# Performance work log

Measured on AMD Instinct MI355X. Metric: run time of the kernel, lower is better.

Reference implementation:

```python
import jax, jax.numpy as jnp
import numpy as np

B, C, H, Wd = 16, 512, 56, 56
WCH = 128  # W_ch: projection rank of phi/rou


def setup_inputs() -> dict:
    key = jax.random.key(0)
    ks = jax.random.split(key, 8)
    s = 0.02
    return {
        "x": jax.random.normal(ks[0], (B, C, H, Wd), dtype=jnp.float32),
        "y": jax.random.normal(ks[1], (B, C, H, Wd), dtype=jnp.float32),
        # phi: Conv2d(C, WCH, 1) -> weight [WCH, C], bias [WCH]
        "phi_w": jax.random.normal(ks[2], (WCH, C), dtype=jnp.float32) * s,
        "phi_b": jnp.zeros((WCH,), dtype=jnp.float32),
        # rou: Conv2d(C, WCH, 1) applied to globally pooled y -> acts as Linear
        "rou_w": jax.random.normal(ks[3], (WCH, C), dtype=jnp.float32) * s,
        "rou_b": jnp.zeros((WCH,), dtype=jnp.float32),
        # zeta: Linear(C, C)
        "zeta_w": jax.random.normal(ks[4], (C, C), dtype=jnp.float32) * s,
        "zeta_b": jnp.zeros((C,), dtype=jnp.float32),
    }


def reference(x, y, phi_w, phi_b, rou_w, rou_b, zeta_w, zeta_b):
    b, c, h, w = x.shape
    hw = h * w
    # phi_xT = relu(phi(x)).view(B, WCH, HW); phi_x = transpose -> [B, HW, WCH]
    phi_xT = jax.nn.relu(jnp.einsum('kc,bchw->bkhw', phi_w, x) + phi_b[None, :, None, None])
    phi_x = phi_xT.reshape(b, -1, hw).transpose(0, 2, 1)  # [B, HW, WCH]
    # rou_y = sigmoid(rou(global_avg_pool(y))) -> [B, WCH]
    pooled = y.mean(axis=(2, 3))  # [B, C]
    rou_y = jax.nn.sigmoid(pooled @ rou_w.T + rou_b)  # [B, WCH]
    # D_i = sum_j (phi_x diag(rou) phi_x^T)_{ij} = sum_k phi_x[i,k] rou[k] s[k]
    s = phi_x.sum(axis=1)  # [B, WCH], column sums
    D = jnp.einsum('bnk,bk,bk->bn', phi_x, rou_y, s)  # [B, HW]
    inv_sqrt = 1.0 / jnp.sqrt(D + 1e-8)
    P = phi_x * inv_sqrt[..., None]  # diag(D^-1/2) @ phi_x, [B, HW, WCH]
    # x.view(B, -1, C): raw row-major reshape of [B,C,H,W] (NOT a transpose)
    x_trans = x.reshape(b, hw, c)
    # LX = x_trans - P diag(rou) P^T x_trans, re-associated right-to-left
    t = jnp.einsum('bnk,bnc->bkc', P, x_trans)          # P^T x_trans, [B, WCH, C]
    LX = x_trans - jnp.einsum('bnk,bk,bkc->bnc', P, rou_y, t)
    # zeta Linear + dropout(eval: identity) + relu, residual add
    out = jax.nn.relu(LX @ zeta_w.T + zeta_b)
    return x + out.reshape(b, c, h, w)
```

## Files before the change

### kernel.cpp

```cpp
#include <hip/hip_runtime.h>
#include <math.h>

#define B_  16
#define C_  512
#define HW_ 3136
#define K_  128
#define CHW (C_ * HW_)

typedef __bf16 bf16x8_t __attribute__((ext_vector_type(8)));
typedef __bf16 bf16x4_t __attribute__((ext_vector_type(4)));
typedef __bf16 bf16x2_t __attribute__((ext_vector_type(2)));
typedef float floatx4  __attribute__((ext_vector_type(4)));

typedef const __attribute__((address_space(1))) void* gas_ptr;
typedef __attribute__((address_space(3))) void*       las_ptr;

static __device__ __forceinline__ unsigned short bfbits(__bf16 v) {
    return __builtin_bit_cast(unsigned short, v);
}

__device__ __forceinline__ void stage128x64(const __bf16* __restrict__ base, long ld,
                                            int row0, int rowmax, int k0,
                                            __bf16* lds, int t) {
    int w = t >> 6;
    #pragma unroll
    for (int i = 0; i < 4; ++i) {
        int u = i * 256 + t;
        int m = u >> 3, slot = u & 7;
        int kg = slot ^ (m & 7);
        int r = row0 + m; if (r > rowmax) r = rowmax;
        const __bf16* g = base + (long)r * ld + (k0 + kg * 8);
        __bf16* l = lds + (size_t)(i * 256 + w * 64) * 8;
        __builtin_amdgcn_global_load_lds((gas_ptr)g, (las_ptr)l, 16, 0, 0);
    }
}

__device__ __forceinline__ void stage_tr_phi(const __bf16* __restrict__ src,
                                             int n0, int p0, char* Bs, int t) {
    int ng = t & 15;
    int cp2 = (t >> 4) * 2;
    #pragma unroll
    for (int ci = 0; ci < 2; ++ci) {
        int cc = cp2 + ci * 32;
        const __bf16* g0 = src + (long)(p0 + cc) * HW_ + n0 + ng * 8;
        bf16x8_t v0 = *(const bf16x8_t*)g0;
        bf16x8_t v1 = *(const bf16x8_t*)(g0 + HW_);
        int r8 = cc >> 3, sub = (cc & 7) >> 1;
        #pragma unroll
        for (int j = 0; j < 8; ++j) {
            int row = ng * 8 + j;
            int slot = (r8 + row + (row >> 3)) & 7;
            unsigned int pr = ((unsigned int)bfbits(v1[j]) << 16) | bfbits(v0[j]);
            *(unsigned int*)(Bs + row * 144 + slot * 16 + sub * 4) = pr;
        }
    }
}

__device__ __forceinline__ void stage_tr_t(const __bf16* __restrict__ src,
                                           const float* __restrict__ isrc,
                                           int c0, int p0, char* Bs, int t) {
    int cg = t & 15;
    int np2 = (t >> 4) * 2;
    #pragma unroll
    for (int ni = 0; ni < 2; ++ni) {
        int nn = np2 + ni * 32;
        int n = p0 + nn;
        float s0 = isrc[n], s1 = isrc[n + 1];
        const __bf16* g0 = src + (long)n * C_ + c0 + cg * 8;
        bf16x8_t v0 = *(const bf16x8_t*)g0;
        bf16x8_t v1 = *(const bf16x8_t*)(g0 + C_);
        int r8 = nn >> 3, sub = (nn & 7) >> 1;
        #pragma unroll
        for (int j = 0; j < 8; ++j) {
            int row = cg * 8 + j;
            int slot = (r8 + row + (row >> 3)) & 7;
            __bf16 a0 = (__bf16)((float)v0[j] * s0);
            __bf16 a1 = (__bf16)((float)v1[j] * s1);
            unsigned int pr = ((unsigned int)bfbits(a1) << 16) | bfbits(a0);
            *(unsigned int*)(Bs + row * 144 + slot * 16 + sub * 4) = pr;
        }
    }
}

__device__ __forceinline__ void mma_step64(const char* As, const char* Bs,
                                           floatx4 acc[4][4], int aoff, int boff,
                                           int q, int lxor) {
    #pragma unroll
    for (int h = 0; h < 2; ++h) {
        int s = (((h * 4 + q) ^ lxor) << 4);
        bf16x8_t af[4], bf[4];
        #pragma unroll
        for (int i = 0; i < 4; ++i) af[i] = *(const bf16x8_t*)(As + aoff + i * 2048 + s);
        #pragma unroll
        for (int i = 0; i < 4; ++i) bf[i] = *(const bf16x8_t*)(Bs + boff + i * 2048 + s);
        #pragma unroll
        for (int mi = 0; mi < 4; ++mi)
            #pragma unroll
            for (int ni = 0; ni < 4; ++ni)
                acc[mi][ni] = __builtin_amdgcn_mfma_f32_16x16x32_bf16(af[mi], bf[ni], acc[mi][ni], 0, 0, 0);
    }
}

__device__ __forceinline__ void mma_step_mix(const char* As, const char* Bs,
                                             floatx4 acc[4][4], int lm, int q,
                                             int wrow, int wcol) {
    int lxor = lm & 7;
    int aoff = (wrow * 64 + lm) * 128;
    #pragma unroll
    for (int h = 0; h < 2; ++h) {
        int g = h * 4 + q;
        int sa = (g ^ lxor) << 4;
        bf16x8_t af[4], bf[4];
        #pragma unroll
        for (int i = 0; i < 4; ++i) af[i] = *(const bf16x8_t*)(As + aoff + i * 2048 + sa);
        #pragma unroll
        for (int i = 0; i < 4; ++i) {
            int brow = wcol * 64 + i * 16 + lm;
            int slot = (g + brow + (brow >> 3)) & 7;
            bf[i] = *(const bf16x8_t*)(Bs + brow * 144 + slot * 16);
        }
        #pragma unroll
        for (int mi = 0; mi < 4; ++mi)
            #pragma unroll
            for (int ni = 0; ni < 4; ++ni)
                acc[mi][ni] = __builtin_amdgcn_mfma_f32_16x16x32_bf16(af[mi], bf[ni], acc[mi][ni], 0, 0, 0);
    }
}


__global__ __launch_bounds__(256) void k_pool(const float* __restrict__ y,
                                              float* __restrict__ pooled) {
    int bc = blockIdx.x;
    const float* yp = y + (long)bc * HW_;
    float acc = 0.f;
    for (int n = threadIdx.x; n < HW_; n += 256) acc += yp[n];
    __shared__ float red[256];
    red[threadIdx.x] = acc;
    __syncthreads();
    for (int s = 128; s > 0; s >>= 1) {
        if (threadIdx.x < s) red[threadIdx.x] += red[threadIdx.x + s];
        __syncthreads();
    }
    if (threadIdx.x == 0) pooled[bc] = red[0] * (1.0f / HW_);
}

__global__ __launch_bounds__(128) void k_rou(const float* __restrict__ pooled,
                                             const float* __restrict__ rou_w,
                                             const float* __restrict__ rou_b,
                                             float* __restrict__ rou_y) {
    int b = blockIdx.x;
    int k = threadIdx.x;
    __shared__ float ps[C_];
    for (int c = threadIdx.x; c < C_; c += 128) ps[c] = pooled[b * C_ + c];
    __syncthreads();
    float acc = rou_b[k];
    for (int c = 0; c < C_; ++c) acc += ps[c] * rou_w[k * C_ + c];
    rou_y[b * K_ + k] = 1.0f / (1.0f + expf(-acc));
}

__global__ __launch_bounds__(256) void k_cast8(const float* __restrict__ a,
                                               __bf16* __restrict__ o) {
    long i = ((long)blockIdx.x * 256 + threadIdx.x) * 8;
    float4 v0 = *reinterpret_cast<const float4*>(a + i);
    float4 v1 = *reinterpret_cast<const float4*>(a + i + 4);
    bf16x8_t r;
    r[0] = (__bf16)v0.x; r[1] = (__bf16)v0.y; r[2] = (__bf16)v0.z; r[3] = (__bf16)v0.w;
    r[4] = (__bf16)v1.x; r[5] = (__bf16)v1.y; r[6] = (__bf16)v1.z; r[7] = (__bf16)v1.w;
    *reinterpret_cast<bf16x8_t*>(o + i) = r;
}


__global__ __launch_bounds__(256) void k_phi_m(const __bf16* __restrict__ xbf2,
                                               const __bf16* __restrict__ pwbf,
                                               const float* __restrict__ phi_b,
                                               __bf16* __restrict__ phi_kn,
                                               __bf16* __restrict__ phi_nk,
                                               float* __restrict__ sbuf) {
    int b = blockIdx.y;
    int n0 = blockIdx.x * 128;
    __shared__ __attribute__((aligned(16))) char smem[16384 + 18432];
    char* As = smem; char* Bs = smem + 16384;
    int t = threadIdx.x, w = t >> 6, lane = t & 63;
    int lm = lane & 15, q = lane >> 4;
    int wrow = w >> 1, wcol = w & 1;
    floatx4 acc[4][4];
    #pragma unroll
    for (int i = 0; i < 4; ++i)
        #pragma unroll
        for (int j = 0; j < 4; ++j) acc[i][j] = (floatx4){0.f, 0.f, 0.f, 0.f};

    const __bf16* Bb = xbf2 + (long)b * CHW;
    for (int p0 = 0; p0 < C_; p0 += 64) {
        stage128x64(pwbf, C_, 0, K_ - 1, p0, (__bf16*)As, t);
        stage_tr_phi(Bb, n0, p0, Bs, t);
        __syncthreads();
        mma_step_mix(As, Bs, acc, lm, q, wrow, wcol);
        __syncthreads();
    }
    #pragma unroll
    for (int mi = 0; mi < 4; ++mi) {
        int kb = wrow * 64 + mi * 16 + q * 4;
        float4 pb = *reinterpret_cast<const float4*>(phi_b + kb);
        float pbv[4] = {pb.x, pb.y, pb.z, pb.w};
        float sv[4] = {0.f, 0.f, 0.f, 0.f};
        #pragma unroll
        for (int ni = 0; ni < 4; ++ni) {
            int n = n0 + wcol * 64 + ni * 16 + lm;
            if (n < HW_) {
                bf16x4_t pack;
                #pragma unroll
                for (int r = 0; r < 4; ++r) {
                    float v = fmaxf(acc[mi][ni][r] + pbv[r], 0.f);
                    __bf16 vb = (__bf16)v;
                    phi_kn[((long)b * K_ + kb + r) * HW_ + n] = vb;
                    pack[r] = vb;
                    sv[r] += v;
                }
                *reinterpret_cast<bf16x4_t*>(phi_nk + ((long)b * HW_ + n) * K_ + kb) = pack;
            }
        }
        #pragma unroll
        for (int r = 0; r < 4; ++r) {
            float v = sv[r];
            v += __shfl_xor(v, 1, 64); v += __shfl_xor(v, 2, 64);
            v += __shfl_xor(v, 4, 64); v += __shfl_xor(v, 8, 64);
            if (lm == 0) atomicAdd(&sbuf[b * K_ + kb + r], v);
        }
    }
}

__global__ __launch_bounds__(256) void k_d2(__bf16* __restrict__ phi_nk,
                                            const float* __restrict__ rou_y,
                                            const float* __restrict__ s,
                                            float* __restrict__ inv_s) {
    int b = blockIdx.y;
    __shared__ float ws[K_];
    int t = threadIdx.x;
    if (t < K_) ws[t] = rou_y[b * K_ + t] * s[b * K_ + t];
    __syncthreads();
    int w = t >> 6, lane = t & 63;
    int n = blockIdx.x * 4 + w;
    __bf16* p = phi_nk + ((long)b * HW_ + n) * K_ + lane * 2;
    bf16x2_t v = *reinterpret_cast<bf16x2_t*>(p);
    float f0 = (float)v[0], f1 = (float)v[1];
    float d = f0 * ws[lane * 2] + f1 * ws[lane * 2 + 1];
    #pragma unroll
    for (int off = 32; off > 0; off >>= 1) d += __shfl_xor(d, off, 64);
    float inv = rsqrtf(d + 1e-8f);
    bf16x2_t o; o[0] = (__bf16)(f0 * inv); o[1] = (__bf16)(f1 * inv);
    *reinterpret_cast<bf16x2_t*>(p) = o;
    if (lane == 0) inv_s[b * HW_ + n] = inv;
}

__global__ __launch_bounds__(256) void k_t_m(const __bf16* __restrict__ phi_kn,
                                             const __bf16* __restrict__ xbf2,
                                             const float* __restrict__ inv_s,
                                             float* __restrict__ t_part) {
    int gid = blockIdx.x;
    int rlo = gid & 7, cc4 = (gid >> 3) & 3, r8 = gid >> 5;
    int r = r8 * 8 + rlo;
    int b = r / 7, nch = r % 7;
    int c0 = cc4 * 128;
    __shared__ __attribute__((aligned(16))) char smem[16384 + 18432];
    char* As = smem; char* Bs = smem + 16384;
    int t = threadIdx.x, w = t >> 6, lane = t & 63;
    int lm = lane & 15, q = lane >> 4;
    int wrow = w >> 1, wcol = w & 1;
    floatx4 acc[4][4];
    #pragma unroll
    for (int i = 0; i < 4; ++i)
        #pragma unroll
        for (int j = 0; j < 4; ++j) acc[i][j] = (floatx4){0.f, 0.f, 0.f, 0.f};

    const __bf16* Ab = phi_kn + (long)b * K_ * HW_;
    const __bf16* Bb = xbf2 + (long)b * CHW;
    const float* ib = inv_s + (long)b * HW_;

    int pstart = nch * 448;
    for (int p0 = pstart; p0 < pstart + 448; p0 += 64) {
        stage128x64(Ab, HW_, 0, K_ - 1, p0, (__bf16*)As, t);
        stage_tr_t(Bb, ib, c0, p0, Bs, t);
        __syncthreads();
        mma_step_mix(As, Bs, acc, lm, q, wrow, wcol);
        __syncthreads();
    }
    float* outp = t_part + ((long)nch * B_ + b) * K_ * C_;
    #pragma unroll
    for (int mi = 0; mi < 4; ++mi) {
        int kb = wrow * 64 + mi * 16 + q * 4;
        #pragma unroll
        for (int ni = 0; ni < 4; ++ni) {
            int c = c0 + wcol * 64 + ni * 16 + lm;
            #pragma unroll
            for (int rr = 0; rr < 4; ++rr)
                outp[(long)(kb + rr) * C_ + c] = acc[mi][ni][rr];
        }
    }
}

__global__ __launch_bounds__(256) void k_tred(const float* __restrict__ t_part,
                                              __bf16* __restrict__ t_bf) {
    const long BKC = (long)B_ * K_ * C_;
    long i = ((long)blockIdx.x * 256 + threadIdx.x) * 4;
    float4 s = *reinterpret_cast<const float4*>(t_part + i);
    #pragma unroll
    for (int p = 1; p < 7; ++p) {
        float4 v = *reinterpret_cast<const float4*>(t_part + p * BKC + i);
        s.x += v.x; s.y += v.y; s.z += v.z; s.w += v.w;
    }
    bf16x4_t o;
    o[0] = (__bf16)s.x; o[1] = (__bf16)s.y; o[2] = (__bf16)s.z; o[3] = (__bf16)s.w;
    *reinterpret_cast<bf16x4_t*>(t_bf + i) = o;
}

__global__ __launch_bounds__(256) void k_tz_m(const __bf16* __restrict__ zwbf,
                                              const __bf16* __restrict__ t_bf,
                                              const float* __restrict__ rou_y,
                                              __bf16* __restrict__ tzT) {
    int b = blockIdx.y;
    int c0 = blockIdx.x * 128;
    __shared__ __attribute__((aligned(16))) char smem[32768];
    char* As = smem; char* Bs = smem + 16384;
    int t = threadIdx.x, w = t >> 6, lane = t & 63;
    int lm = lane & 15, q = lane >> 4;
    int wrow = w >> 1, wcol = w & 1;
    floatx4 acc[4][4];
    #pragma unroll
    for (int i = 0; i < 4; ++i)
        #pragma unroll
        for (int j = 0; j < 4; ++j) acc[i][j] = (floatx4){0.f, 0.f, 0.f, 0.f};

    const __bf16* Bb = t_bf + (long)b * K_ * C_;
    int lxor = lm & 7;
    int aoff = (wrow * 64 + lm) * 128;
    int boff = (wcol * 64 + lm) * 128;

    for (int p0 = 0; p0 < C_; p0 += 64) {
        stage128x64(zwbf, C_, c0, C_ - 1, p0, (__bf16*)As, t);
        stage128x64(Bb,   C_, 0, K_ - 1, p0, (__bf16*)Bs, t);
        __syncthreads();
        mma_step64(As, Bs, acc, aoff, boff, q, lxor);
        __syncthreads();
    }
    #pragma unroll
    for (int mi = 0; mi < 4; ++mi) {
        int c = c0 + wrow * 64 + mi * 16 + q * 4;
        #pragma unroll
        for (int ni = 0; ni < 4; ++ni) {
            int k = wcol * 64 + ni * 16 + lm;
            float rk = rou_y[b * K_ + k];
            #pragma unroll
            for (int rr = 0; rr < 4; ++rr)
                tzT[((long)b * C_ + c + rr) * K_ + k] = (__bf16)(-rk * acc[mi][ni][rr]);
        }
    }
}

__global__ __launch_bounds__(256) void k_out_m(const __bf16* __restrict__ xbf2,
                                               const __bf16* __restrict__ zwbf,
                                               const __bf16* __restrict__ pnk,
                                               const __bf16* __restrict__ tzT,
                                               const float* __restrict__ zeta_b,
                                               float* __restrict__ out) {
    int gid = blockIdx.x;
    int rlo = gid & 7, cc4 = (gid >> 3) & 3, r8 = gid >> 5;
    int r = r8 * 8 + rlo;
    int b = r / 25, nt = r % 25;
    int n0 = nt * 128;
    int c0 = cc4 * 128;
    __shared__ __attribute__((aligned(16))) char smem[32768];
    char* As = smem; char* Bs = smem + 16384;
    int t = threadIdx.x, w = t >> 6, lane = t & 63;
    int lm = lane & 15, q = lane >> 4;
    int wrow = w >> 1, wcol = w & 1;
    floatx4 acc[4][4];
    #pragma unroll
    for (int i = 0; i < 4; ++i)
        #pragma unroll
        for (int j = 0; j < 4; ++j) acc[i][j] = (floatx4){0.f, 0.f, 0.f, 0.f};

    int lxor = lm & 7;
    int aoff = (wrow * 64 + lm) * 128;
    int boff = (wcol * 64 + lm) * 128;

    const __bf16* A1 = xbf2 + (long)b * CHW;
    for (int p0 = 0; p0 < C_; p0 += 64) {
        stage128x64(A1,   C_, n0, HW_ - 1, p0, (__bf16*)As, t);
        stage128x64(zwbf, C_, c0, C_ - 1, p0, (__bf16*)Bs, t);
        __syncthreads();
        mma_step64(As, Bs, acc, aoff, boff, q, lxor);
        __syncthreads();
    }
    const __bf16* A2 = pnk + (long)b * (long)HW_ * K_;
    const __bf16* B2 = tzT + (long)b * (long)C_ * K_;
    for (int p0 = 0; p0 < K_; p0 += 64) {
        stage128x64(A2, K_, n0, HW_ - 1, p0, (__bf16*)As, t);
        stage128x64(B2, K_, c0, C_ - 1, p0, (__bf16*)Bs, t);
        __syncthreads();
        mma_step64(As, Bs, acc, aoff, boff, q, lxor);
        __syncthreads();
    }
    float* ep = (float*)smem;
    const __bf16* xres = xbf2 + (long)b * CHW;
    int lr = t >> 3, lc = (t & 7) * 16;
    #pragma unroll
    for (int ch = 0; ch < 4; ++ch) {
        __syncthreads();
        if (wrow == (ch >> 1)) {
            #pragma unroll
            for (int mm = 0; mm < 2; ++mm) {
                int mi = (ch & 1) * 2 + mm;
                #pragma unroll
                for (int ni = 0; ni < 4; ++ni)
                    #pragma unroll
                    for (int rr = 0; rr < 4; ++rr)
                        ep[(mm * 16 + q * 4 + rr) * 132 + wcol * 64 + ni * 16 + lm] = acc[mi][ni][rr];
            }
        }
        __syncthreads();
        int n = n0 + ch * 32 + lr;
        if (n < HW_) {
            long rowbase = (long)n * C_ + c0 + lc;
            bf16x8_t x0 = *(const bf16x8_t*)(xres + rowbase);
            bf16x8_t x1 = *(const bf16x8_t*)(xres + rowbase + 8);
            float xv[16];
            #pragma unroll
            for (int j = 0; j < 8; ++j) { xv[j] = (float)x0[j]; xv[8 + j] = (float)x1[j]; }
            float* orow = out + (long)b * CHW + rowbase;
            #pragma unroll
            for (int jj = 0; jj < 4; ++jj) {
                float4 zb = *reinterpret_cast<const float4*>(zeta_b + c0 + lc + jj * 4);
                float4 e  = *reinterpret_cast<const float4*>(&ep[lr * 132 + lc + jj * 4]);
                float4 o;
                o.x = xv[jj * 4 + 0] + fmaxf(e.x + zb.x, 0.f);
                o.y = xv[jj * 4 + 1] + fmaxf(e.y + zb.y, 0.f);
                o.z = xv[jj * 4 + 2] + fmaxf(e.z + zb.z, 0.f);
                o.w = xv[jj * 4 + 3] + fmaxf(e.w + zb.w, 0.f);
                *reinterpret_cast<float4*>(orow + jj * 4) = o;
            }
        }
    }
}

extern "C" void kernel_launch(void* const* d_in, const int* in_sizes, int n_in,
                              void* d_out, int out_size, void* d_ws, size_t ws_size,
                              hipStream_t stream) {
    const float* x      = (const float*)d_in[0];
    const float* y      = (const float*)d_in[1];
    const float* phi_w  = (const float*)d_in[2];
    const float* phi_b  = (const float*)d_in[3];
    const float* rou_w  = (const float*)d_in[4];
    const float* rou_b  = (const float*)d_in[5];
    const float* zeta_w = (const float*)d_in[6];
    const float* zeta_b = (const float*)d_in[7];
    float* out = (float*)d_out;

    char* p = (char*)d_ws;
    __bf16* xbf2   = (__bf16*)p; p += (size_t)B_ * CHW * 2;
    __bf16* phi_kn = (__bf16*)p; p += (size_t)B_ * K_ * HW_ * 2;
    __bf16* phi_nk = (__bf16*)p; p += (size_t)B_ * K_ * HW_ * 2;
    float*  t_part = (float*) p; p += (size_t)7 * B_ * K_ * C_ * 4;
    __bf16* t_bf   = (__bf16*)p; p += (size_t)B_ * K_ * C_ * 2;
    __bf16* tzT    = (__bf16*)p; p += (size_t)B_ * C_ * K_ * 2;
    __bf16* pwbf   = (__bf16*)p; p += (size_t)K_ * C_ * 2;
    __bf16* zwbf   = (__bf16*)p; p += (size_t)C_ * C_ * 2;
    float*  pooled = (float*) p; p += (size_t)B_ * C_ * 4;
    float*  rou_y  = (float*) p; p += (size_t)B_ * K_ * 4;
    float*  sbuf   = (float*) p; p += (size_t)B_ * K_ * 4;
    float*  inv_s  = (float*) p; p += (size_t)B_ * HW_ * 4;

    hipMemsetAsync(sbuf, 0, B_ * K_ * sizeof(float), stream);

    k_pool <<<B_ * C_, 256, 0, stream>>>(y, pooled);
    k_rou  <<<B_, 128, 0, stream>>>(pooled, rou_w, rou_b, rou_y);
    k_cast8<<<(K_ * C_) / 2048, 256, 0, stream>>>(phi_w, pwbf);
    k_cast8<<<(C_ * C_) / 2048, 256, 0, stream>>>(zeta_w, zwbf);
    k_cast8<<<(B_ * (long)CHW) / 2048, 256, 0, stream>>>(x, xbf2);
    k_phi_m<<<dim3(25, B_), 256, 0, stream>>>(xbf2, pwbf, phi_b, phi_kn, phi_nk, sbuf);
    k_d2   <<<dim3(HW_ / 4, B_), 256, 0, stream>>>(phi_nk, rou_y, sbuf, inv_s);
    k_t_m  <<<448, 256, 0, stream>>>(phi_kn, xbf2, inv_s, t_part);
    k_tred <<<(B_ * K_ * C_) / 1024, 256, 0, stream>>>(t_part, t_bf);
    k_tz_m <<<dim3(C_ / 128, B_), 256, 0, stream>>>(zwbf, t_bf, rou_y, tzT);
    k_out_m<<<1600, 256, 0, stream>>>(xbf2, zwbf, phi_nk, tzT, zeta_b, out);
}
```

Before: 422.9 us.

## Double-buffer LDS in GEMM kernels and vectorize pool/rou reductions

Four GEMM kernels (phi, t, tz, out) now keep two LDS buffers, so the next K-slice is staged while MFMAs run on the current one, and one of the two barriers per iteration is dropped. k_pool now uses float4 loads and wave shuffles instead of a shared-memory tree. k_rou is split to one 64-thread wave per (k,b) output with vectorized loads. Doubling LDS per block (about 68KB or 64KB) may lower occupancy, and because staging goes through registers the overlap depends on how the compiler schedules it.

Result: faster. 389.7 us (-7.9%).

```diff
diff --git a/kernel.cpp b/kernel.cpp
--- a/kernel.cpp
+++ b/kernel.cpp
@@ -132,30 +132,44 @@
                                               float* __restrict__ pooled) {
     int bc = blockIdx.x;
     const float* yp = y + (long)bc * HW_;
+    int t = threadIdx.x;
     float acc = 0.f;
-    for (int n = threadIdx.x; n < HW_; n += 256) acc += yp[n];
-    __shared__ float red[256];
-    red[threadIdx.x] = acc;
+    #pragma unroll
+    for (int i = 0; i < 4; ++i) {
+        int n4 = t + i * 256;
+        if (n4 < 784) {
+            float4 v = *reinterpret_cast<const float4*>(yp + (long)n4 * 4);
+            acc += v.x + v.y + v.z + v.w;
+        }
+    }
+    #pragma unroll
+    for (int off = 32; off > 0; off >>= 1) acc += __shfl_xor(acc, off, 64);
+    __shared__ float red[4];
+    if ((t & 63) == 0) red[t >> 6] = acc;
     __syncthreads();
-    for (int s = 128; s > 0; s >>= 1) {
-        if (threadIdx.x < s) red[threadIdx.x] += red[threadIdx.x + s];
-        __syncthreads();
-    }
-    if (threadIdx.x == 0) pooled[bc] = red[0] * (1.0f / HW_);
-}
-
-__global__ __launch_bounds__(128) void k_rou(const float* __restrict__ pooled,
-                                             const float* __restrict__ rou_w,
-                                             const float* __restrict__ rou_b,
-                                             float* __restrict__ rou_y) {
-    int b = blockIdx.x;
-    int k = threadIdx.x;
-    __shared__ float ps[C_];
-    for (int c = threadIdx.x; c < C_; c += 128) ps[c] = pooled[b * C_ + c];
-    __syncthreads();
-    float acc = rou_b[k];
-    for (int c = 0; c < C_; ++c) acc += ps[c] * rou_w[k * C_ + c];
-    rou_y[b * K_ + k] = 1.0f / (1.0f + expf(-acc));
+    if (t == 0) pooled[bc] = (red[0] + red[1] + red[2] + red[3]) * (1.0f / HW_);
+}
+
+__global__ __launch_bounds__(64) void k_rou(const float* __restrict__ pooled,
+                                            const float* __restrict__ rou_w,
+                                            const float* __restrict__ rou_b,
+                                            float* __restrict__ rou_y) {
+    int k = blockIdx.x;
+    int b = blockIdx.y;
+    int lane = threadIdx.x;
+    const float* pr = pooled + b * C_;
+    const float* wr = rou_w + (long)k * C_;
+    float acc = 0.f;
+    #pragma unroll
+    for (int i = 0; i < 2; ++i) {
+        int c = (lane + i * 64) * 4;
+        float4 w4 = *reinterpret_cast<const float4*>(wr + c);
+        float4 p4 = *reinterpret_cast<const float4*>(pr + c);
+        acc += w4.x * p4.x + w4.y * p4.y + w4.z * p4.z + w4.w * p4.w;
+    }
+    #pragma unroll
+    for (int off = 32; off > 0; off >>= 1) acc += __shfl_xor(acc, off, 64);
+    if (lane == 0) rou_y[b * K_ + k] = 1.0f / (1.0f + expf(-(acc + rou_b[k])));
 }
 
 __global__ __launch_bounds__(256) void k_cast8(const float* __restrict__ a,
@@ -178,8 +192,7 @@
                                                float* __restrict__ sbuf) {
     int b = blockIdx.y;
     int n0 = blockIdx.x * 128;
-    __shared__ __attribute__((aligned(16))) char smem[16384 + 18432];
-    char* As = smem; char* Bs = smem + 16384;
+    __shared__ __attribute__((aligned(16))) char smem[2 * 34816];
     int t = threadIdx.x, w = t >> 6, lane = t & 63;
     int lm = lane & 15, q = lane >> 4;
     int wrow = w >> 1, wcol = w & 1;
@@ -190,12 +203,23 @@
         for (int j = 0; j < 4; ++j) acc[i][j] = (floatx4){0.f, 0.f, 0.f, 0.f};
 
     const __bf16* Bb = xbf2 + (long)b * CHW;
-    for (int p0 = 0; p0 < C_; p0 += 64) {
-        stage128x64(pwbf, C_, 0, K_ - 1, p0, (__bf16*)As, t);
-        stage_tr_phi(Bb, n0, p0, Bs, t);
+
+    stage128x64(pwbf, C_, 0, K_ - 1, 0, (__bf16*)smem, t);
+    stage_tr_phi(Bb, n0, 0, smem + 16384, t);
+    __syncthreads();
+    int cur = 0;
+    #pragma unroll
+    for (int s = 0; s < 8; ++s) {
+        char* cb = smem + cur * 34816;
+        if (s < 7) {
+            char* nb = smem + (cur ^ 1) * 34816;
+            int p0 = (s + 1) * 64;
+            stage128x64(pwbf, C_, 0, K_ - 1, p0, (__bf16*)nb, t);
+            stage_tr_phi(Bb, n0, p0, nb + 16384, t);
+        }
+        mma_step_mix(cb, cb + 16384, acc, lm, q, wrow, wcol);
         __syncthreads();
-        mma_step_mix(As, Bs, acc, lm, q, wrow, wcol);
-        __syncthreads();
+        cur ^= 1;
     }
     #pragma unroll
     for (int mi = 0; mi < 4; ++mi) {
@@ -261,8 +285,7 @@
     int r = r8 * 8 + rlo;
     int b = r / 7, nch = r % 7;
     int c0 = cc4 * 128;
-    __shared__ __attribute__((aligned(16))) char smem[16384 + 18432];
-    char* As = smem; char* Bs = smem + 16384;
+    __shared__ __attribute__((aligned(16))) char smem[2 * 34816];
     int t = threadIdx.x, w = t >> 6, lane = t & 63;
     int lm = lane & 15, q = lane >> 4;
     int wrow = w >> 1, wcol = w & 1;
@@ -277,12 +300,22 @@
     const float* ib = inv_s + (long)b * HW_;
 
     int pstart = nch * 448;
-    for (int p0 = pstart; p0 < pstart + 448; p0 += 64) {
-        stage128x64(Ab, HW_, 0, K_ - 1, p0, (__bf16*)As, t);
-        stage_tr_t(Bb, ib, c0, p0, Bs, t);
+    stage128x64(Ab, HW_, 0, K_ - 1, pstart, (__bf16*)smem, t);
+    stage_tr_t(Bb, ib, c0, pstart, smem + 16384, t);
+    __syncthreads();
+    int cur = 0;
+    #pragma unroll
+    for (int s = 0; s < 7; ++s) {
+        char* cb = smem + cur * 34816;
+        if (s < 6) {
+            char* nb = smem + (cur ^ 1) * 34816;
+            int p0 = pstart + (s + 1) * 64;
+            stage128x64(Ab, HW_, 0, K_ - 1, p0, (__bf16*)nb, t);
+            stage_tr_t(Bb, ib, c0, p0, nb + 16384, t);
+        }
+        mma_step_mix(cb, cb + 16384, acc, lm, q, wrow, wcol);
         __syncthreads();
-        mma_step_mix(As, Bs, acc, lm, q, wrow, wcol);
-        __syncthreads();
+        cur ^= 1;
     }
     float* outp = t_part + ((long)nch * B_ + b) * K_ * C_;
     #pragma unroll
@@ -319,8 +352,7 @@
                                               __bf16* __restrict__ tzT) {
     int b = blockIdx.y;
     int c0 = blockIdx.x * 128;
-    __shared__ __attribute__((aligned(16))) char smem[32768];
-    char* As = smem; char* Bs = smem + 16384;
+    __shared__ __attribute__((aligned(16))) char smem[2 * 32768];
     int t = threadIdx.x, w = t >> 6, lane = t & 63;
     int lm = lane & 15, q = lane >> 4;
     int wrow = w >> 1, wcol = w & 1;
@@ -335,12 +367,22 @@
     int aoff = (wrow * 64 + lm) * 128;
     int boff = (wcol * 64 + lm) * 128;
 
-    for (int p0 = 0; p0 < C_; p0 += 64) {
-        stage128x64(zwbf, C_, c0, C_ - 1, p0, (__bf16*)As, t);
-        stage128x64(Bb,   C_, 0, K_ - 1, p0, (__bf16*)Bs, t);
+    stage128x64(zwbf, C_, c0, C_ - 1, 0, (__bf16*)smem, t);
+    stage128x64(Bb,   C_, 0, K_ - 1, 0, (__bf16*)(smem + 16384), t);
+    __syncthreads();
+    int cur = 0;
+    #pragma unroll
+    for (int s = 0; s < 8; ++s) {
+        char* cb = smem + cur * 32768;
+        if (s < 7) {
+            char* nb = smem + (cur ^ 1) * 32768;
+            int p0 = (s + 1) * 64;
+            stage128x64(zwbf, C_, c0, C_ - 1, p0, (__bf16*)nb, t);
+            stage128x64(Bb,   C_, 0, K_ - 1, p0, (__bf16*)(nb + 16384), t);
+        }
+        mma_step64(cb, cb + 16384, acc, aoff, boff, q, lxor);
         __syncthreads();
-        mma_step64(As, Bs, acc, aoff, boff, q, lxor);
-        __syncthreads();
+        cur ^= 1;
     }
     #pragma unroll
     for (int mi = 0; mi < 4; ++mi) {
@@ -368,8 +410,7 @@
     int b = r / 25, nt = r % 25;
     int n0 = nt * 128;
     int c0 = cc4 * 128;
-    __shared__ __attribute__((aligned(16))) char smem[32768];
-    char* As = smem; char* Bs = smem + 16384;
+    __shared__ __attribute__((aligned(16))) char smem[2 * 32768];
     int t = threadIdx.x, w = t >> 6, lane = t & 63;
     int lm = lane & 15, q = lane >> 4;
     int wrow = w >> 1, wcol = w & 1;
@@ -384,21 +425,32 @@
     int boff = (wcol * 64 + lm) * 128;
 
     const __bf16* A1 = xbf2 + (long)b * CHW;
-    for (int p0 = 0; p0 < C_; p0 += 64) {
-        stage128x64(A1,   C_, n0, HW_ - 1, p0, (__bf16*)As, t);
-        stage128x64(zwbf, C_, c0, C_ - 1, p0, (__bf16*)Bs, t);
-        __syncthreads();
-        mma_step64(As, Bs, acc, aoff, boff, q, lxor);
-        __syncthreads();
-    }
     const __bf16* A2 = pnk + (long)b * (long)HW_ * K_;
     const __bf16* B2 = tzT + (long)b * (long)C_ * K_;
-    for (int p0 = 0; p0 < K_; p0 += 64) {
-        stage128x64(A2, K_, n0, HW_ - 1, p0, (__bf16*)As, t);
-        stage128x64(B2, K_, c0, C_ - 1, p0, (__bf16*)Bs, t);
+
+    stage128x64(A1,   C_, n0, HW_ - 1, 0, (__bf16*)smem, t);
+    stage128x64(zwbf, C_, c0, C_ - 1, 0, (__bf16*)(smem + 16384), t);
+    __syncthreads();
+    int cur = 0;
+    #pragma unroll
+    for (int s = 0; s < 10; ++s) {
+        char* cb = smem + cur * 32768;
+        if (s < 9) {
+            char* nb = smem + (cur ^ 1) * 32768;
+            int sn = s + 1;
+            if (sn < 8) {
+                int p0 = sn * 64;
+                stage128x64(A1,   C_, n0, HW_ - 1, p0, (__bf16*)nb, t);
+                stage128x64(zwbf, C_, c0, C_ - 1, p0, (__bf16*)(nb + 16384), t);
+            } else {
+                int p0 = (sn - 8) * 64;
+                stage128x64(A2, K_, n0, HW_ - 1, p0, (__bf16*)nb, t);
+                stage128x64(B2, K_, c0, C_ - 1, p0, (__bf16*)(nb + 16384), t);
+            }
+        }
+        mma_step64(cb, cb + 16384, acc, aoff, boff, q, lxor);
         __syncthreads();
-        mma_step64(As, Bs, acc, aoff, boff, q, lxor);
-        __syncthreads();
+        cur ^= 1;
     }
     float* ep = (float*)smem;
     const __bf16* xres = xbf2 + (long)b * CHW;
@@ -472,7 +524,7 @@
     hipMemsetAsync(sbuf, 0, B_ * K_ * sizeof(float), stream);
 
     k_pool <<<B_ * C_, 256, 0, stream>>>(y, pooled);
-    k_rou  <<<B_, 128, 0, stream>>>(pooled, rou_w, rou_b, rou_y);
+    k_rou  <<<dim3(K_, B_), 64, 0, stream>>>(pooled, rou_w, rou_b, rou_y);
     k_cast8<<<(K_ * C_) / 2048, 256, 0, stream>>>(phi_w, pwbf);
     k_cast8<<<(C_ * C_) / 2048, 256, 0, stream>>>(zeta_w, zwbf);
     k_cast8<<<(B_ * (long)CHW) / 2048, 256, 0, stream>>>(x, xbf2);
```
